# Kernel optimization log

Hardware: AMD Instinct MI355X
Metric: run time of the kernel (lower is better)

The kernel has to match this reference:

```python
import jax, jax.numpy as jnp
import numpy as np

N_NODES = 50000
N_EDGES = 800000
DIM = 128
BN_EPS = 1e-5
GATE_EPS = 1e-6


def setup_inputs() -> dict:
    key = jax.random.key(0)
    ks = jax.random.split(key, 14)
    scale = 1.0 / np.sqrt(DIM)
    inp = {
        "h": jax.random.normal(ks[0], (N_NODES, DIM), dtype=jnp.float32),
        "e": jax.random.normal(ks[1], (N_EDGES, DIM), dtype=jnp.float32),
        "src": jax.random.randint(ks[2], (N_EDGES,), 0, N_NODES),
        "dst": jax.random.randint(ks[3], (N_EDGES,), 0, N_NODES),
        # Linear A, B, D, E (n_mlp_layer=1 -> single Linear each)
        "Wa": jax.random.uniform(ks[4], (DIM, DIM), jnp.float32, -scale, scale),
        "ba": jax.random.uniform(ks[5], (DIM,), jnp.float32, -scale, scale),
        "Wb": jax.random.uniform(ks[6], (DIM, DIM), jnp.float32, -scale, scale),
        "bb": jax.random.uniform(ks[7], (DIM,), jnp.float32, -scale, scale),
        "Wd": jax.random.uniform(ks[8], (DIM, DIM), jnp.float32, -scale, scale),
        "bd": jax.random.uniform(ks[9], (DIM,), jnp.float32, -scale, scale),
        "We": jax.random.uniform(ks[10], (DIM, DIM), jnp.float32, -scale, scale),
        "be": jax.random.uniform(ks[11], (DIM,), jnp.float32, -scale, scale),
        # BatchNorm1d affine params (fresh init: gamma=1, beta=0)
        "gamma": jnp.ones((DIM,), jnp.float32),
        "beta": jnp.zeros((DIM,), jnp.float32),
    }
    return inp


def reference(h, e, src, dst, Wa, ba, Wb, bb, Wd, bd, We, be, gamma, beta):
    N = h.shape[0]
    # dense node projections
    Ah = h @ Wa + ba
    Bh = h @ Wb + bb
    Dh = h @ Wd + bd
    Eh = h @ We + be
    # edge gather + sigmoid gate: e_ij = Dh[src] + Eh[dst]
    sigma = jax.nn.sigmoid(Dh[src] + Eh[dst])          # [E, D]
    # scatter-sum by destination node (variable degree)
    num = jax.ops.segment_sum(sigma * Bh[src], dst, num_segments=N)
    den = jax.ops.segment_sum(sigma, dst, num_segments=N) + GATE_EPS
    h_new = Ah + num / den
    # BatchNorm1d (training mode: biased batch statistics) + relu
    mean = jnp.mean(h_new, axis=0)
    var = jnp.mean(jnp.square(h_new - mean), axis=0)
    h_new = (h_new - mean) * jax.lax.rsqrt(var + BN_EPS) * gamma + beta
    h_new = jax.nn.relu(h_new)
    # residual=False (default), dropout=0.0 -> identity
    return h_new, e
```

## Files before the change

kernel.cpp:

```cpp
#include <hip/hip_runtime.h>
#include <hip/hip_bf16.h>

#define DIM 128
#define GATE_EPS 1e-6f
#define BN_EPS 1e-5f

typedef unsigned int u32;
typedef unsigned short u16;

__device__ __forceinline__ float bflo(u32 u) { return __uint_as_float(u << 16); }
__device__ __forceinline__ float bfhi(u32 u) { return __uint_as_float(u & 0xffff0000u); }

__device__ __forceinline__ u16 f2bf(float f) {
    u32 u = __float_as_uint(f);
    u32 r = (u + 0x7fffu + ((u >> 16) & 1u)) >> 16;
    return (u16)r;
}

__device__ __forceinline__ float loadF(const void* p, size_t i, int bf) {
    if (bf) return __uint_as_float(((u32)((const u16*)p)[i]) << 16);
    return ((const float*)p)[i];
}

__global__ void detect_dtype(const void* __restrict__ h, int* __restrict__ flag) {
    if (threadIdx.x == 0 && blockIdx.x == 0) {
        const u16* us = (const u16*)h;
        int cnt = 0;
        for (int i = 0; i < 256; ++i) {
            int e8 = (us[2 * i] >> 7) & 0xFF;
            if (e8 >= 0x60 && e8 <= 0x8F) ++cnt;
        }
        *flag = (cnt >= 192) ? 1 : 0;
    }
}

__global__ __launch_bounds__(256) void proj_gemm(
    const void* __restrict__ h,
    const void* __restrict__ W0, const void* __restrict__ b0,
    const void* __restrict__ W1, const void* __restrict__ b1,
    const void* __restrict__ W2, const void* __restrict__ b2,
    const void* __restrict__ W3, const void* __restrict__ b3,
    float* __restrict__ oAh, u32* __restrict__ oDB, u32* __restrict__ oEhb,
    int N, const int* __restrict__ flagp)
{
    const void* W; const void* bias;
    switch (blockIdx.y) {
        case 0:  W = W0; bias = b0; break;
        case 1:  W = W1; bias = b1; break;
        case 2:  W = W2; bias = b2; break;
        default: W = W3; bias = b3; break;
    }
    const int bf = *flagp;

    __shared__ float Hs[64][DIM + 4];
    __shared__ float Ws[16][DIM];

    const int t  = threadIdx.x;
    const int m0 = blockIdx.x * 64;

    if (bf) {
        for (int f = t; f < 1024; f += 256) {
            int r = f >> 4, c8 = f & 15;
            int gr = m0 + r;
            uint4 v = make_uint4(0u, 0u, 0u, 0u);
            if (gr < N) v = ((const uint4*)h)[(size_t)gr * 16 + c8];
            float* p = &Hs[r][c8 * 8];
            p[0] = bflo(v.x); p[1] = bfhi(v.x);
            p[2] = bflo(v.y); p[3] = bfhi(v.y);
            p[4] = bflo(v.z); p[5] = bfhi(v.z);
            p[6] = bflo(v.w); p[7] = bfhi(v.w);
        }
    } else {
        for (int f = t; f < 2048; f += 256) {
            int r = f >> 5, c4 = f & 31;
            int gr = m0 + r;
            float4 v = make_float4(0.f, 0.f, 0.f, 0.f);
            if (gr < N) v = ((const float4*)h)[(size_t)gr * 32 + c4];
            float* p = &Hs[r][c4 * 4];
            p[0] = v.x; p[1] = v.y; p[2] = v.z; p[3] = v.w;
        }
    }

    const int cg = t & 31;
    const int rg = t >> 5;

    float acc[8][4];
    #pragma unroll
    for (int i = 0; i < 8; ++i)
        #pragma unroll
        for (int j = 0; j < 4; ++j) acc[i][j] = 0.f;

    for (int kc = 0; kc < DIM; kc += 16) {
        __syncthreads();
        if (bf) {
            int r = t >> 4, c8 = t & 15;
            uint4 v = ((const uint4*)W)[(size_t)(kc + r) * 16 + c8];
            float* p = &Ws[r][c8 * 8];
            p[0] = bflo(v.x); p[1] = bfhi(v.x);
            p[2] = bflo(v.y); p[3] = bfhi(v.y);
            p[4] = bflo(v.z); p[5] = bfhi(v.z);
            p[6] = bflo(v.w); p[7] = bfhi(v.w);
        } else {
            for (int f = t; f < 512; f += 256) {
                int r = f >> 5, c4 = f & 31;
                float4 v = ((const float4*)W)[(size_t)(kc + r) * 32 + c4];
                float* p = &Ws[r][c4 * 4];
                p[0] = v.x; p[1] = v.y; p[2] = v.z; p[3] = v.w;
            }
        }
        __syncthreads();
        #pragma unroll
        for (int kk = 0; kk < 16; ++kk) {
            float4 w = *((const float4*)&Ws[kk][cg * 4]);
            #pragma unroll
            for (int i = 0; i < 8; ++i) {
                float hv = Hs[rg * 8 + i][kc + kk];
                acc[i][0] += hv * w.x;
                acc[i][1] += hv * w.y;
                acc[i][2] += hv * w.z;
                acc[i][3] += hv * w.w;
            }
        }
    }

    float bv[4];
    #pragma unroll
    for (int j = 0; j < 4; ++j) bv[j] = loadF(bias, cg * 4 + j, bf);

    const int y = blockIdx.y;
    #pragma unroll
    for (int i = 0; i < 8; ++i) {
        int gr = m0 + rg * 8 + i;
        if (gr < N) {
            float v0 = acc[i][0] + bv[0];
            float v1 = acc[i][1] + bv[1];
            float v2 = acc[i][2] + bv[2];
            float v3 = acc[i][3] + bv[3];
            if (y == 0) {
                ((float4*)oAh)[(size_t)gr * 32 + cg] = make_float4(v0, v1, v2, v3);
            } else {
                uint2 p;
                p.x = (u32)f2bf(v0) | ((u32)f2bf(v1) << 16);
                p.y = (u32)f2bf(v2) | ((u32)f2bf(v3) << 16);
                size_t idx;
                if (y == 1)      idx = (size_t)gr * 64 + 32 + cg;
                else if (y == 2) idx = (size_t)gr * 64 + cg;
                else             idx = (size_t)gr * 32 + cg;
                u32* base = (y == 3) ? oEhb : oDB;
                ((uint2*)base)[idx] = p;
            }
        }
    }
}

__global__ __launch_bounds__(256) void k_hist(const int* __restrict__ dst,
                                              int* __restrict__ deg, int E)
{
    int e = blockIdx.x * 256 + threadIdx.x;
    if (e < E) atomicAdd(&deg[dst[e]], 1);
}

__global__ __launch_bounds__(256) void k_scan1(const int* __restrict__ deg,
                                               int* __restrict__ rowstart,
                                               int* __restrict__ part, int N)
{
    __shared__ int s[256];
    int t = threadIdx.x;
    int i = blockIdx.x * 256 + t;
    int d = (i < N) ? deg[i] : 0;
    s[t] = d;
    __syncthreads();
    for (int off = 1; off < 256; off <<= 1) {
        int v = (t >= off) ? s[t - off] : 0;
        __syncthreads();
        s[t] += v;
        __syncthreads();
    }
    if (i < N) rowstart[i] = s[t] - d;
    if (t == 255) part[blockIdx.x] = s[255];
}

__global__ void k_scan2(int* __restrict__ part, int nb)
{
    __shared__ int s[256];
    int t = threadIdx.x;
    int d = (t < nb) ? part[t] : 0;
    s[t] = d;
    __syncthreads();
    for (int off = 1; off < 256; off <<= 1) {
        int v = (t >= off) ? s[t - off] : 0;
        __syncthreads();
        s[t] += v;
        __syncthreads();
    }
    if (t < nb) part[t] = s[t] - d;
}

__global__ __launch_bounds__(256) void k_scan3(int* __restrict__ rowstart,
                                               int* __restrict__ cursor,
                                               const int* __restrict__ part,
                                               int N, int E)
{
    int i = blockIdx.x * 256 + threadIdx.x;
    if (i < N) {
        int v = rowstart[i] + part[blockIdx.x];
        rowstart[i] = v;
        cursor[i] = v;
    }
    if (i == 0) rowstart[N] = E;
}

__global__ __launch_bounds__(256) void k_scatter(const int* __restrict__ src,
                                                 const int* __restrict__ dst,
                                                 int* __restrict__ cursor,
                                                 int* __restrict__ esrc, int E)
{
    int e = blockIdx.x * 256 + threadIdx.x;
    if (e < E) {
        int pos = atomicAdd(&cursor[dst[e]], 1);
        esrc[pos] = src[e];
    }
}

__global__ __launch_bounds__(256) void k_aggregate(
    const float* __restrict__ Ah, const u32* __restrict__ DB,
    const u32* __restrict__ Ehb,
    const int* __restrict__ rowstart, const int* __restrict__ esrc,
    float* __restrict__ hnew, float* __restrict__ gsum, float* __restrict__ gsq,
    int N)
{
    int t = threadIdx.x;
    int lane = t & 63;
    int wv = t >> 6;
    int nquads = (N + 3) >> 2;

    float lsum0 = 0.f, lsum1 = 0.f, lsq0 = 0.f, lsq1 = 0.f;
    for (int q = blockIdx.x; q < nquads; q += gridDim.x) {
        int n = q * 4 + wv;
        if (n < N) {
            u32 ehp = Ehb[(size_t)n * 64 + lane];
            float eh0 = bflo(ehp), eh1 = bfhi(ehp);
            float2 ahp = ((const float2*)Ah)[(size_t)n * 64 + lane];
            float num0 = 0.f, den0 = 0.f, num1 = 0.f, den1 = 0.f;
            int beg = rowstart[n], end = rowstart[n + 1];
            int k = beg;
            for (; k + 2 <= end; k += 2) {
                int s0 = esrc[k], s1 = esrc[k + 1];
                u32 dh0 = DB[(size_t)s0 * 128 + lane];
                u32 bh0 = DB[(size_t)s0 * 128 + 64 + lane];
                u32 dh1 = DB[(size_t)s1 * 128 + lane];
                u32 bh1 = DB[(size_t)s1 * 128 + 64 + lane];
                float sa0 = 1.f / (1.f + __expf(-(bflo(dh0) + eh0)));
                float sa1 = 1.f / (1.f + __expf(-(bfhi(dh0) + eh1)));
                float sb0 = 1.f / (1.f + __expf(-(bflo(dh1) + eh0)));
                float sb1 = 1.f / (1.f + __expf(-(bfhi(dh1) + eh1)));
                num0 = fmaf(sa0, bflo(bh0), num0); den0 += sa0;
                num1 = fmaf(sa1, bfhi(bh0), num1); den1 += sa1;
                num0 = fmaf(sb0, bflo(bh1), num0); den0 += sb0;
                num1 = fmaf(sb1, bfhi(bh1), num1); den1 += sb1;
            }
            if (k < end) {
                int s0 = esrc[k];
                u32 dh0 = DB[(size_t)s0 * 128 + lane];
                u32 bh0 = DB[(size_t)s0 * 128 + 64 + lane];
                float sa0 = 1.f / (1.f + __expf(-(bflo(dh0) + eh0)));
                float sa1 = 1.f / (1.f + __expf(-(bfhi(dh0) + eh1)));
                num0 = fmaf(sa0, bflo(bh0), num0); den0 += sa0;
                num1 = fmaf(sa1, bfhi(bh0), num1); den1 += sa1;
            }
            float x0 = ahp.x + num0 / (den0 + GATE_EPS);
            float x1 = ahp.y + num1 / (den1 + GATE_EPS);
            ((float2*)hnew)[(size_t)n * 64 + lane] = make_float2(x0, x1);
            lsum0 += x0; lsq0 += x0 * x0;
            lsum1 += x1; lsq1 += x1 * x1;
        }
    }
    __shared__ float S0[256], S1[256], Q0[256], Q1[256];
    S0[t] = lsum0; S1[t] = lsum1; Q0[t] = lsq0; Q1[t] = lsq1;
    __syncthreads();
    if (t < 64) {
        float s0 = S0[t] + S0[t + 64] + S0[t + 128] + S0[t + 192];
        float s1 = S1[t] + S1[t + 64] + S1[t + 128] + S1[t + 192];
        float q0 = Q0[t] + Q0[t + 64] + Q0[t + 128] + Q0[t + 192];
        float q1 = Q1[t] + Q1[t + 64] + Q1[t + 128] + Q1[t + 192];
        atomicAdd(&gsum[2 * t],     s0);
        atomicAdd(&gsum[2 * t + 1], s1);
        atomicAdd(&gsq[2 * t],      q0);
        atomicAdd(&gsq[2 * t + 1],  q1);
    }
}

__global__ void bn_finalize(const float* __restrict__ gsum, const float* __restrict__ gsq,
                            const void* __restrict__ gamma, const void* __restrict__ beta,
                            float* __restrict__ scale, float* __restrict__ shift,
                            int N, const int* __restrict__ flagp)
{
    int c = threadIdx.x;
    int bf = *flagp;
    if (c < DIM) {
        float invn = 1.f / (float)N;
        float mean = gsum[c] * invn;
        float var  = fmaxf(gsq[c] * invn - mean * mean, 0.f);
        float g = loadF(gamma, c, bf);
        float b = loadF(beta, c, bf);
        float sc = rsqrtf(var + BN_EPS) * g;
        scale[c] = sc;
        shift[c] = b - mean * sc;
    }
}

__global__ __launch_bounds__(256) void bn_apply(
    const float* __restrict__ hnew, const float* __restrict__ scale,
    const float* __restrict__ shift, void* __restrict__ outh,
    int total, const int* __restrict__ flagp)
{
    __shared__ float s_sc[DIM], s_sh[DIM];
    int t = threadIdx.x;
    if (t < DIM) { s_sc[t] = scale[t]; s_sh[t] = shift[t]; }
    __syncthreads();
    int bf = *flagp;

    int idx = blockIdx.x * 256 + t;
    int stride = gridDim.x * 256;
    for (int i = idx; i < total; i += stride) {
        int c = i & 127;
        float x = fmaxf(0.f, hnew[i] * s_sc[c] + s_sh[c]);
        if (bf) ((u16*)outh)[i] = f2bf(x);
        else    ((float*)outh)[i] = x;
    }
}

__global__ __launch_bounds__(256) void copy_e(
    const void* __restrict__ e, void* __restrict__ dout,
    size_t nd, size_t ecount, const int* __restrict__ flagp)
{
    int bf = *flagp;
    size_t esz = bf ? 2 : 4;
    const uint4* s = (const uint4*)e;
    uint4* d = (uint4*)((char*)dout + nd * esz);
    size_t n16 = (ecount * esz) / 16;
    size_t idx = (size_t)blockIdx.x * 256 + threadIdx.x;
    size_t stride = (size_t)gridDim.x * 256;
    for (size_t i = idx; i < n16; i += stride) d[i] = s[i];
}

extern "C" void kernel_launch(void* const* d_in, const int* in_sizes, int n_in,
                              void* d_out, int out_size, void* d_ws, size_t ws_size,
                              hipStream_t stream)
{
    const void* h     = d_in[0];
    const void* e     = d_in[1];
    const int*  src   = (const int*)d_in[2];
    const int*  dst   = (const int*)d_in[3];
    const void* Wa    = d_in[4];
    const void* ba    = d_in[5];
    const void* Wb    = d_in[6];
    const void* bb    = d_in[7];
    const void* Wd    = d_in[8];
    const void* bd    = d_in[9];
    const void* We    = d_in[10];
    const void* be    = d_in[11];
    const void* gamma = d_in[12];
    const void* beta  = d_in[13];

    const int N = in_sizes[0] / DIM;
    const int E = in_sizes[2];
    const size_t nd = (size_t)N * DIM;
    const size_t ecount = (size_t)E * DIM;

    float* ws    = (float*)d_ws;
    float* Ah    = ws;
    float* hnew  = ws + nd;
    u32*   DB    = (u32*)(ws + 2 * nd);
    u32*   Ehb   = (u32*)(ws + 3 * nd);
    float* gsum  = ws + 3 * nd + nd / 2;
    float* gsq   = gsum + DIM;
    float* scale = gsum + 2 * DIM;
    float* shift = gsum + 3 * DIM;
    int*   flag  = (int*)(gsum + 4 * DIM);
    int*   deg      = flag + 64;
    int*   rowstart = deg + N;
    int*   cursor   = rowstart + N + 1;
    int*   part     = cursor + N;
    int*   esrc     = part + 256;

    detect_dtype<<<1, 64, 0, stream>>>(h, flag);

    hipMemsetAsync(gsum, 0, 4 * DIM * sizeof(float), stream);
    hipMemsetAsync(deg, 0, (size_t)N * sizeof(int), stream);

    const int nbE = (E + 255) / 256;
    const int nbN = (N + 255) / 256;

    k_hist<<<nbE, 256, 0, stream>>>(dst, deg, E);
    k_scan1<<<nbN, 256, 0, stream>>>(deg, rowstart, part, N);
    k_scan2<<<1, 256, 0, stream>>>(part, nbN);
    k_scan3<<<nbN, 256, 0, stream>>>(rowstart, cursor, part, N, E);
    k_scatter<<<nbE, 256, 0, stream>>>(src, dst, cursor, esrc, E);

    dim3 g1((N + 63) / 64, 4);
    proj_gemm<<<g1, 256, 0, stream>>>(h, Wa, ba, Wb, bb, Wd, bd, We, be,
                                      Ah, DB, Ehb, N, flag);

    k_aggregate<<<2048, 256, 0, stream>>>(Ah, DB, Ehb, rowstart, esrc,
                                          hnew, gsum, gsq, N);

    bn_finalize<<<1, 128, 0, stream>>>(gsum, gsq, gamma, beta, scale, shift, N, flag);

    bn_apply<<<2048, 256, 0, stream>>>(hnew, scale, shift, d_out, (int)nd, flag);

    copy_e<<<4096, 256, 0, stream>>>(e, d_out, nd, ecount, flag);
}
```

Before: 549.2 us.

## Compute node projections with bf16 MFMA, verify samples, fall back to old GEMM

Replaces the shared-memory scalar projection GEMM with a bf16 MFMA kernel that reads h and a pre-transposed, packed copy of the four weight matrices directly from global memory. A small kernel spot-checks sampled outputs against a scalar recomputation, and the old GEMM (now k_repair) exits early unless that check fails. This aims to cut projection compute time on the matrix cores. In exchange it adds three launches and assumes bf16 inputs unconditionally, relying on the verify-and-repair path when the inputs are fp32.

```diff
diff --git a/kernel.cpp b/kernel.cpp
--- a/kernel.cpp
+++ b/kernel.cpp
@@ -7,6 +7,9 @@
 
 typedef unsigned int u32;
 typedef unsigned short u16;
+
+typedef __attribute__((ext_vector_type(8))) short short8v;
+typedef __attribute__((ext_vector_type(4))) float f32x4;
 
 __device__ __forceinline__ float bflo(u32 u) { return __uint_as_float(u << 16); }
 __device__ __forceinline__ float bfhi(u32 u) { return __uint_as_float(u & 0xffff0000u); }
@@ -15,6 +18,10 @@
     u32 u = __float_as_uint(f);
     u32 r = (u + 0x7fffu + ((u >> 16) & 1u)) >> 16;
     return (u16)r;
+}
+
+__device__ __forceinline__ float bf2f(u16 v) {
+    return __uint_as_float(((u32)v) << 16);
 }
 
 __device__ __forceinline__ float loadF(const void* p, size_t i, int bf) {
@@ -34,15 +41,128 @@
     }
 }
 
-__global__ __launch_bounds__(256) void proj_gemm(
+__global__ __launch_bounds__(256) void k_transposeW(
+    const u16* __restrict__ W0, const u16* __restrict__ W1,
+    const u16* __restrict__ W2, const u16* __restrict__ W3,
+    u32* __restrict__ Wt32)
+{
+    int p = blockIdx.x;
+    const u16* W = (p == 0) ? W0 : (p == 1) ? W1 : (p == 2) ? W2 : W3;
+    int t = threadIdx.x;
+    for (int i = t; i < 8192; i += 256) {
+        int c = i >> 6;
+        int g = i & 63;
+        u16 lo = W[(2 * g) * DIM + c];
+        u16 hi = W[(2 * g + 1) * DIM + c];
+        Wt32[p * 8192 + i] = (u32)lo | ((u32)hi << 16);
+    }
+}
+
+__global__ __launch_bounds__(256) void mfma_proj(
+    const u16* __restrict__ h, const u16* __restrict__ Wt,
+    const u16* __restrict__ b0, const u16* __restrict__ b1,
+    const u16* __restrict__ b2, const u16* __restrict__ b3,
+    float* __restrict__ Ah, u16* __restrict__ DBu, u16* __restrict__ Ehbu,
+    int N)
+{
+    const int p  = blockIdx.y >> 1;
+    const int ch = blockIdx.y & 1;
+    const u16* bias = (p == 0) ? b0 : (p == 1) ? b1 : (p == 2) ? b2 : b3;
+
+    const int t = threadIdx.x;
+    const int l = t & 63;
+    const int w = t >> 6;
+    const int m0 = blockIdx.x * 64 + w * 16;
+
+    int row_a = m0 + (l & 15);
+    int rowc = (row_a < N) ? row_a : (N - 1);
+    const u16* hp = h + (size_t)rowc * DIM + ((l >> 4) * 8);
+    short8v a0 = *(const short8v*)(hp + 0);
+    short8v a1 = *(const short8v*)(hp + 32);
+    short8v a2 = *(const short8v*)(hp + 64);
+    short8v a3 = *(const short8v*)(hp + 96);
+
+    const int ln16 = l & 15;
+    const int kgrp = (l >> 4) * 8;
+
+    #pragma unroll
+    for (int ct = 0; ct < 4; ++ct) {
+        const int ccol = ch * 64 + ct * 16 + ln16;
+        const u16* wp = Wt + ((size_t)(p * DIM + ccol)) * DIM + kgrp;
+        short8v q0 = *(const short8v*)(wp + 0);
+        short8v q1 = *(const short8v*)(wp + 32);
+        short8v q2 = *(const short8v*)(wp + 64);
+        short8v q3 = *(const short8v*)(wp + 96);
+
+        f32x4 acc = {0.f, 0.f, 0.f, 0.f};
+        acc = __builtin_amdgcn_mfma_f32_16x16x32_bf16(a0, q0, acc, 0, 0, 0);
+        acc = __builtin_amdgcn_mfma_f32_16x16x32_bf16(a1, q1, acc, 0, 0, 0);
+        acc = __builtin_amdgcn_mfma_f32_16x16x32_bf16(a2, q2, acc, 0, 0, 0);
+        acc = __builtin_amdgcn_mfma_f32_16x16x32_bf16(a3, q3, acc, 0, 0, 0);
+
+        float bv = bf2f(bias[ccol]);
+
+        #pragma unroll
+        for (int r = 0; r < 4; ++r) {
+            int row = m0 + (l >> 4) * 4 + r;
+            if (row < N) {
+                float v = acc[r] + bv;
+                if (p == 0)      Ah[(size_t)row * DIM + ccol] = v;
+                else if (p == 1) DBu[(size_t)row * 256 + 128 + ccol] = f2bf(v);
+                else if (p == 2) DBu[(size_t)row * 256 + ccol] = f2bf(v);
+                else             Ehbu[(size_t)row * DIM + ccol] = f2bf(v);
+            }
+        }
+    }
+}
+
+__global__ __launch_bounds__(256) void k_verify(
+    const u16* __restrict__ h,
+    const u16* __restrict__ Wa, const u16* __restrict__ Wb,
+    const u16* __restrict__ Wd, const u16* __restrict__ We,
+    const u16* __restrict__ ba, const u16* __restrict__ bb,
+    const u16* __restrict__ bd, const u16* __restrict__ be,
+    const float* __restrict__ Ah, const u16* __restrict__ DBu,
+    const u16* __restrict__ Ehbu,
+    int N, int* __restrict__ okp)
+{
+    __shared__ int nbad;
+    int t = threadIdx.x;
+    if (t == 0) nbad = 0;
+    __syncthreads();
+    for (int s = 0; s < 2; ++s) {
+        int idx = t + s * 256;
+        int p = idx & 3;
+        int r = (int)(((long long)idx * 1999 + 17) % N);
+        int c = (idx * 37 + 5) & 127;
+        const u16* W  = (p == 0) ? Wa : (p == 1) ? Wb : (p == 2) ? Wd : We;
+        const u16* bi = (p == 0) ? ba : (p == 1) ? bb : (p == 2) ? bd : be;
+        float acc = 0.f;
+        for (int k = 0; k < DIM; ++k)
+            acc += bf2f(h[(size_t)r * DIM + k]) * bf2f(W[(size_t)k * DIM + c]);
+        acc += bf2f(bi[c]);
+        float got;
+        if (p == 0)      got = Ah[(size_t)r * DIM + c];
+        else if (p == 1) got = bf2f(DBu[(size_t)r * 256 + 128 + c]);
+        else if (p == 2) got = bf2f(DBu[(size_t)r * 256 + c]);
+        else             got = bf2f(Ehbu[(size_t)r * DIM + c]);
+        if (fabsf(got - acc) > 0.08f) atomicAdd(&nbad, 1);
+    }
+    __syncthreads();
+    if (t == 0) okp[0] = (nbad == 0) ? 1 : 0;
+}
+
+__global__ __launch_bounds__(256) void k_repair(
     const void* __restrict__ h,
     const void* __restrict__ W0, const void* __restrict__ b0,
     const void* __restrict__ W1, const void* __restrict__ b1,
     const void* __restrict__ W2, const void* __restrict__ b2,
     const void* __restrict__ W3, const void* __restrict__ b3,
     float* __restrict__ oAh, u32* __restrict__ oDB, u32* __restrict__ oEhb,
-    int N, const int* __restrict__ flagp)
-{
+    int N, const int* __restrict__ flagp, const int* __restrict__ okp)
+{
+    if (okp[0]) return;
+
     const void* W; const void* bias;
     switch (blockIdx.y) {
         case 0:  W = W0; bias = b0; break;
@@ -377,7 +497,8 @@
     float* gsq   = gsum + DIM;
     float* scale = gsum + 2 * DIM;
     float* shift = gsum + 3 * DIM;
-    int*   flag  = (int*)(gsum + 4 * DIM);
+    u32*   Wt32  = (u32*)(gsum + 4 * DIM);
+    int*   flag  = (int*)(Wt32 + 4 * 8192);
     int*   deg      = flag + 64;
     int*   rowstart = deg + N;
     int*   cursor   = rowstart + N + 1;
@@ -398,9 +519,26 @@
     k_scan3<<<nbN, 256, 0, stream>>>(rowstart, cursor, part, N, E);
     k_scatter<<<nbE, 256, 0, stream>>>(src, dst, cursor, esrc, E);
 
-    dim3 g1((N + 63) / 64, 4);
-    proj_gemm<<<g1, 256, 0, stream>>>(h, Wa, ba, Wb, bb, Wd, bd, We, be,
-                                      Ah, DB, Ehb, N, flag);
+    k_transposeW<<<4, 256, 0, stream>>>((const u16*)Wa, (const u16*)Wb,
+                                        (const u16*)Wd, (const u16*)We, Wt32);
+
+    dim3 gm((N + 63) / 64, 8);
+    mfma_proj<<<gm, 256, 0, stream>>>((const u16*)h, (const u16*)Wt32,
+                                      (const u16*)ba, (const u16*)bb,
+                                      (const u16*)bd, (const u16*)be,
+                                      Ah, (u16*)DB, (u16*)Ehb, N);
+
+    k_verify<<<1, 256, 0, stream>>>((const u16*)h,
+                                    (const u16*)Wa, (const u16*)Wb,
+                                    (const u16*)Wd, (const u16*)We,
+                                    (const u16*)ba, (const u16*)bb,
+                                    (const u16*)bd, (const u16*)be,
+                                    Ah, (const u16*)DB, (const u16*)Ehb,
+                                    N, flag + 1);
+
+    dim3 gr((N + 63) / 64, 4);
+    k_repair<<<gr, 256, 0, stream>>>(h, Wa, ba, Wb, bb, Wd, bd, We, be,
+                                     Ah, DB, Ehb, N, flag, flag + 1);
 
     k_aggregate<<<2048, 256, 0, stream>>>(Ah, DB, Ehb, rowstart, esrc,
                                           hnew, gsum, gsq, N);
```

New measurement: 616.8 us. 12.3% more time.
